# Performance work log

Measured on AMD Instinct MI355X. Metric: run time of the kernel, lower is better.

## Reference

```python
import jax, jax.numpy as jnp
import numpy as np

N = 100000
E = 1600000
F_IN, H = 64, 128


def setup_inputs() -> dict:
    key = jax.random.key(0)
    ks = jax.random.split(key, 8)
    inp = {
        "x": jax.random.normal(ks[0], (N, F_IN), dtype=jnp.float32),
        "edge_index": jax.random.randint(ks[1], (2, E), 0, N, dtype=jnp.int64),
        "W1": jax.random.normal(ks[2], (F_IN, H), dtype=jnp.float32) / np.sqrt(F_IN),
        "b1": jnp.zeros((H,), jnp.float32),
        "W2": jax.random.normal(ks[3], (H, H), dtype=jnp.float32) / np.sqrt(H),
        "b2": jnp.zeros((H,), jnp.float32),
        "W3": jax.random.normal(ks[4], (H, H // 2), dtype=jnp.float32) / np.sqrt(H),
        "b3": jnp.zeros((H // 2,), jnp.float32),
        "Wc1": jax.random.normal(ks[5], (H // 2, H // 4), dtype=jnp.float32) / np.sqrt(H // 2),
        "bc1": jnp.zeros((H // 4,), jnp.float32),
        "Wc2": jax.random.normal(ks[6], (H // 4, 2), dtype=jnp.float32) / np.sqrt(H // 4),
        "bc2": jnp.zeros((2,), jnp.float32),
    }
    return inp


def _gcn_norm(edge_index, n):
    # PyG GCNConv default: add self-loops, symmetric D^-1/2 A_hat D^-1/2 norm
    loop = jnp.arange(n, dtype=edge_index.dtype)
    src = jnp.concatenate([edge_index[0], loop])
    dst = jnp.concatenate([edge_index[1], loop])
    deg = jax.ops.segment_sum(jnp.ones_like(dst, dtype=jnp.float32), dst, num_segments=n)
    dis = jax.lax.rsqrt(jnp.maximum(deg, 1.0))
    norm = dis[src] * dis[dst]  # [E+N]
    return src, dst, norm


def _gcn_conv(x, W, b, src, dst, norm, n):
    h = x @ W                      # [N, H_out]
    msg = h[src] * norm[:, None]   # gather + scale, [E+N, H_out]
    out = jax.ops.segment_sum(msg, dst, num_segments=n)  # scatter-add
    return out + b


def reference(x, edge_index, W1, b1, W2, b2, W3, b3, Wc1, bc1, Wc2, bc2):
    n = x.shape[0]
    src, dst, norm = _gcn_norm(edge_index, n)
    h1 = jax.nn.relu(_gcn_conv(x, W1, b1, src, dst, norm, n))
    h2 = jax.nn.relu(_gcn_conv(h1, W2, b2, src, dst, norm, n))
    h3 = jax.nn.relu(_gcn_conv(h2, W3, b3, src, dst, norm, n))
    pooled = jnp.mean(h3, axis=0, keepdims=True)  # [1, H//2]
    z = jax.nn.relu(pooled @ Wc1 + bc1)
    logits = z @ Wc2 + bc2
    return jax.nn.softmax(logits, axis=1)
```

## Files before the change

kernel.cpp:

```cpp
#include <hip/hip_runtime.h>

#define NN 100000
#define NE 1600000
#define NBUCKET 391
#define CHUNK 4096

typedef __attribute__((ext_vector_type(2))) float v2f;
typedef __attribute__((ext_vector_type(8))) short bf16x8;
typedef __attribute__((ext_vector_type(4))) float f32x4;


__device__ __forceinline__ unsigned int pk4fp8(float a, float b, float c, float d) {
    int t = __builtin_amdgcn_cvt_pk_fp8_f32(a, b, 0, false);
    t = __builtin_amdgcn_cvt_pk_fp8_f32(c, d, t, true);
    return (unsigned int)t;
}
__device__ __forceinline__ void acc4(unsigned int u, float* a) {
    v2f p0 = __builtin_amdgcn_cvt_pk_f32_fp8((int)u, false);
    v2f p1 = __builtin_amdgcn_cvt_pk_f32_fp8((int)u, true);
    a[0] += p0.x; a[1] += p0.y; a[2] += p1.x; a[3] += p1.y;
}
__device__ __forceinline__ void acc16(uint4 u, float* a) {
    acc4(u.x, a); acc4(u.y, a + 4); acc4(u.z, a + 8); acc4(u.w, a + 12);
}


__device__ __forceinline__ unsigned short f2b(float f) {
    unsigned int u; __builtin_memcpy(&u, &f, 4);
    unsigned int r = (u + 0x7fffu + ((u >> 16) & 1u)) >> 16;
    return (unsigned short)r;
}
__device__ __forceinline__ unsigned int pk2b(float a, float b) {
    return (unsigned int)f2b(a) | ((unsigned int)f2b(b) << 16);
}

__global__ __launch_bounds__(256) void k_init(
    const float* __restrict__ W1, const float* __restrict__ W2,
    const float* __restrict__ W3, uint4* __restrict__ Wp,
    int* __restrict__ bcnt) {
    int t = blockIdx.x * 256 + threadIdx.x;
    if (t < 4096) {
        const float* W; int Dout, e, base;
        if (t < 1024)       { W = W1; Dout = 128; e = t;        base = 0; }
        else if (t < 3072)  { W = W2; Dout = 128; e = t - 1024; base = 1024; }
        else                { W = W3; Dout = 64;  e = t - 3072; base = 3072; }
        int k4q = e / Dout, ch = e % Dout;
        int k0 = (k4q >> 2) * 32 + (k4q & 3) * 8;
        float v[8];
        #pragma unroll
        for (int j = 0; j < 8; j++) v[j] = W[(k0 + j) * Dout + ch];
        uint4 u;
        u.x = pk2b(v[0], v[1]); u.y = pk2b(v[2], v[3]);
        u.z = pk2b(v[4], v[5]); u.w = pk2b(v[6], v[7]);
        Wp[base + e] = u;
    } else {
        int i = t - 4096;
        if (i < NBUCKET) bcnt[i] = 0;
    }
}


__global__ __launch_bounds__(256) void k_p1(const int* __restrict__ dst,
                                            int* __restrict__ bcnt, int E) {
    __shared__ int h[NBUCKET];
    for (int i = threadIdx.x; i < NBUCKET; i += 256) h[i] = 0;
    __syncthreads();
    int stride = gridDim.x * 256;
    for (int i = blockIdx.x * 256 + threadIdx.x; i < E; i += stride)
        atomicAdd(&h[dst[i] >> 8], 1);
    __syncthreads();
    for (int i = threadIdx.x; i < NBUCKET; i += 256)
        if (h[i]) atomicAdd(&bcnt[i], h[i]);
}

__global__ void k_scanb(const int* __restrict__ bcnt, int* __restrict__ bbase,
                        int* __restrict__ bfill) {
    __shared__ int s[512];
    int t = threadIdx.x;
    int v = (t < NBUCKET) ? bcnt[t] : 0;
    s[t] = v; __syncthreads();
    for (int off = 1; off < 512; off <<= 1) {
        int x = (t >= off) ? s[t - off] : 0;
        __syncthreads();
        s[t] += x;
        __syncthreads();
    }
    if (t < NBUCKET) { int ex = s[t] - v; bbase[t] = ex; bfill[t] = ex; }
    if (t == NBUCKET) bbase[t] = s[511];
}

__global__ __launch_bounds__(256) void k_p2(const int* __restrict__ src,
                                            const int* __restrict__ dst,
                                            int* __restrict__ bfill,
                                            unsigned int* __restrict__ entries, int E) {
    __shared__ int h[NBUCKET];
    __shared__ int cur[NBUCKET];
    int c0 = blockIdx.x * CHUNK;
    int c1 = min(E, c0 + CHUNK);
    for (int i = threadIdx.x; i < NBUCKET; i += 256) h[i] = 0;
    __syncthreads();
    for (int i = c0 + threadIdx.x; i < c1; i += 256) atomicAdd(&h[dst[i] >> 8], 1);
    __syncthreads();
    for (int i = threadIdx.x; i < NBUCKET; i += 256)
        cur[i] = h[i] ? atomicAdd(&bfill[i], h[i]) : 0;
    __syncthreads();
    for (int i = c0 + threadIdx.x; i < c1; i += 256) {
        int d = dst[i];
        int bkt = d >> 8;
        int pos = atomicAdd(&cur[bkt], 1);
        entries[pos] = (unsigned int)src[i] | ((unsigned int)(d & 255) << 17);
    }
}

__global__ __launch_bounds__(256) void k_p4x(const unsigned int* __restrict__ entries,
                                             const int* __restrict__ bbase,
                                             int* __restrict__ row_ptr,
                                             float* __restrict__ dis,
                                             int* __restrict__ col,
                                             const float4* __restrict__ x4,
                                             uint2* __restrict__ xb2, int N) {
    __shared__ int cnt[256];
    __shared__ int cur[256];
    __shared__ int sc[256];
    __shared__ float sdis[256];
    int b = blockIdx.x;
    int e0 = bbase[b], e1 = bbase[b + 1];
    int t = threadIdx.x;
    cnt[t] = 0; __syncthreads();
    for (int i = e0 + t; i < e1; i += 256)
        atomicAdd(&cnt[(entries[i] >> 17) & 255], 1);
    __syncthreads();
    int v = cnt[t];
    sc[t] = v; __syncthreads();
    for (int off = 1; off < 256; off <<= 1) {
        int x = (t >= off) ? sc[t - off] : 0;
        __syncthreads();
        sc[t] += x;
        __syncthreads();
    }
    int ex = sc[t] - v;
    int n = (b << 8) + t;
    float dv = rsqrtf((float)(v + 1));
    if (n <= N) row_ptr[n] = e0 + ex;
    if (n < N) dis[n] = dv;
    sdis[t] = dv;
    cur[t] = e0 + ex;
    __syncthreads();
    for (int i = e0 + t; i < e1; i += 256) {
        unsigned int en = entries[i];
        int pos = atomicAdd(&cur[(en >> 17) & 255], 1);
        col[pos] = (int)(en & 0x1FFFF);
    }
    for (int idx = t; idx < 256 * 8; idx += 256) {
        int node = idx >> 3, k = idx & 7;
        int gn = (b << 8) + node;
        if (gn < N) {
            float s = sdis[node];
            float4 A = x4[gn * 16 + 2 * k];
            float4 B = x4[gn * 16 + 2 * k + 1];
            uint2 u;
            u.x = pk4fp8(A.x * s, A.y * s, A.z * s, A.w * s);
            u.y = pk4fp8(B.x * s, B.y * s, B.z * s, B.w * s);
            xb2[gn * 8 + k] = u;
        }
    }
}

__global__ __launch_bounds__(256) void k_l1f(
    const uint4* __restrict__ xb4, const int* __restrict__ row_ptr,
    const int* __restrict__ col, const float* __restrict__ dis,
    const uint4* __restrict__ Wp, const float* __restrict__ b1,
    unsigned int* __restrict__ h1u, int N) {
    __shared__ unsigned short lds[4][16][72];
    const int tid = threadIdx.x, lane = tid & 63, wave = tid >> 6;
    const int slot = lane >> 2, seg = lane & 3;
    const int n = blockIdx.x * 64 + wave * 16 + slot;
    float a[16];
    #pragma unroll
    for (int q = 0; q < 16; q++) a[q] = 0.f;
    if (n < N) {
        int b = row_ptr[n], e = row_ptr[n + 1];
        acc16(xb4[n * 4 + seg], a);
        int i = b;
        for (; i + 4 <= e; i += 4) {
            int c0 = col[i], c1 = col[i + 1], c2 = col[i + 2], c3 = col[i + 3];
            uint4 u0 = xb4[c0 * 4 + seg], u1 = xb4[c1 * 4 + seg];
            uint4 u2 = xb4[c2 * 4 + seg], u3 = xb4[c3 * 4 + seg];
            acc16(u0, a); acc16(u1, a); acc16(u2, a); acc16(u3, a);
        }
        for (; i < e; i++) acc16(xb4[col[i] * 4 + seg], a);
        float s = dis[n];
        #pragma unroll
        for (int q = 0; q < 16; q++) a[q] *= s;
    }
    uint4 u0, u1;
    u0.x = pk2b(a[0],  a[1]);  u0.y = pk2b(a[2],  a[3]);
    u0.z = pk2b(a[4],  a[5]);  u0.w = pk2b(a[6],  a[7]);
    u1.x = pk2b(a[8],  a[9]);  u1.y = pk2b(a[10], a[11]);
    u1.z = pk2b(a[12], a[13]); u1.w = pk2b(a[14], a[15]);
    *(uint4*)&lds[wave][slot][seg * 16]     = u0;
    *(uint4*)&lds[wave][slot][seg * 16 + 8] = u1;
    __syncthreads();
    const int quad = lane >> 4, l16 = lane & 15;
    const int node = blockIdx.x * 64 + wave * 16 + l16;
    const bool valid = node < N;
    bf16x8 bfrag[2];
    #pragma unroll
    for (int kt = 0; kt < 2; kt++)
        bfrag[kt] = *(bf16x8*)&lds[wave][l16][kt * 32 + quad * 8];
    const float s2 = valid ? dis[node] : 0.f;
    #pragma unroll
    for (int ct = 0; ct < 8; ct++) {
        f32x4 c = {0.f, 0.f, 0.f, 0.f};
        #pragma unroll
        for (int kt = 0; kt < 2; kt++) {
            uint4 wu = Wp[(kt * 4 + quad) * 128 + ct * 16 + l16];
            c = __builtin_amdgcn_mfma_f32_16x16x32_bf16(*(bf16x8*)&wu, bfrag[kt], c, 0, 0, 0);
        }
        if (valid) {
            const int chb = ct * 16 + quad * 4;
            float r0 = fmaxf(c[0] + b1[chb + 0], 0.f) * s2;
            float r1 = fmaxf(c[1] + b1[chb + 1], 0.f) * s2;
            float r2 = fmaxf(c[2] + b1[chb + 2], 0.f) * s2;
            float r3 = fmaxf(c[3] + b1[chb + 3], 0.f) * s2;
            h1u[(size_t)node * 32 + ct * 4 + quad] = pk4fp8(r0, r1, r2, r3);
        }
    }
}

__global__ __launch_bounds__(256) void k_agg128s(
    const uint4* __restrict__ g4, const int* __restrict__ row_ptr,
    const int* __restrict__ col, const float* __restrict__ dis,
    uint4* __restrict__ outb, int N) {
    int tid = threadIdx.x;
    int lane = tid & 63, wave = tid >> 6;
    int slot = lane >> 3, seg = lane & 7;
    int n = blockIdx.x * 32 + wave * 8 + slot;
    if (n >= N) return;
    int b = row_ptr[n], e = row_ptr[n + 1];
    float a[16];
    #pragma unroll
    for (int q = 0; q < 16; q++) a[q] = 0.f;
    acc16(g4[n * 8 + seg], a);
    int i = b;
    for (; i + 4 <= e; i += 4) {
        int c0 = col[i], c1 = col[i + 1], c2 = col[i + 2], c3 = col[i + 3];
        uint4 u0 = g4[c0 * 8 + seg], u1 = g4[c1 * 8 + seg];
        uint4 u2 = g4[c2 * 8 + seg], u3 = g4[c3 * 8 + seg];
        acc16(u0, a); acc16(u1, a); acc16(u2, a); acc16(u3, a);
    }
    for (; i < e; i++) acc16(g4[col[i] * 8 + seg], a);
    float s = dis[n];
    uint4 u0, u1;
    u0.x = pk2b(s*a[0],  s*a[1]);  u0.y = pk2b(s*a[2],  s*a[3]);
    u0.z = pk2b(s*a[4],  s*a[5]);  u0.w = pk2b(s*a[6],  s*a[7]);
    u1.x = pk2b(s*a[8],  s*a[9]);  u1.y = pk2b(s*a[10], s*a[11]);
    u1.z = pk2b(s*a[12], s*a[13]); u1.w = pk2b(s*a[14], s*a[15]);
    outb[n * 16 + seg * 2]     = u0;
    outb[n * 16 + seg * 2 + 1] = u1;
}

__global__ __launch_bounds__(256) void k_mm23(
    const uint4* __restrict__ Xb,
    const uint4* __restrict__ Wp2, const uint4* __restrict__ Wp3,
    const float* __restrict__ b2, const float* __restrict__ dis,
    unsigned int* __restrict__ g3u, int N) {
    __shared__ unsigned short lds[4][16][136];
    const int tid = threadIdx.x, lane = tid & 63, wave = tid >> 6;
    const int quad = lane >> 4, l16 = lane & 15;
    const int node = blockIdx.x * 64 + wave * 16 + l16;
    const bool valid = node < N;
    const int nc = valid ? node : (N - 1);
    bf16x8 bfrag[4];
    const uint4* xrow = Xb + (size_t)nc * 16;
    #pragma unroll
    for (int kt = 0; kt < 4; kt++) {
        uint4 u = xrow[kt * 4 + quad];
        bfrag[kt] = *(bf16x8*)&u;
    }
    const float s = valid ? dis[node] : 0.f;
    #pragma unroll
    for (int ct = 0; ct < 8; ct++) {
        f32x4 c = {0.f, 0.f, 0.f, 0.f};
        #pragma unroll
        for (int kt = 0; kt < 4; kt++) {
            uint4 wu = Wp2[(kt * 4 + quad) * 128 + ct * 16 + l16];
            c = __builtin_amdgcn_mfma_f32_16x16x32_bf16(*(bf16x8*)&wu, bfrag[kt], c, 0, 0, 0);
        }
        const int chb = ct * 16 + quad * 4;
        float r0 = fmaxf(c[0] + b2[chb + 0], 0.f) * s;
        float r1 = fmaxf(c[1] + b2[chb + 1], 0.f) * s;
        float r2 = fmaxf(c[2] + b2[chb + 2], 0.f) * s;
        float r3 = fmaxf(c[3] + b2[chb + 3], 0.f) * s;
        uint2 u; u.x = pk2b(r0, r1); u.y = pk2b(r2, r3);
        *(uint2*)&lds[wave][l16][chb] = u;
    }
    __syncthreads();
    bf16x8 b2frag[4];
    #pragma unroll
    for (int kt = 0; kt < 4; kt++)
        b2frag[kt] = *(bf16x8*)&lds[wave][l16][kt * 32 + quad * 8];
    #pragma unroll
    for (int ct = 0; ct < 4; ct++) {
        f32x4 c = {0.f, 0.f, 0.f, 0.f};
        #pragma unroll
        for (int kt = 0; kt < 4; kt++) {
            uint4 wu = Wp3[(kt * 4 + quad) * 64 + ct * 16 + l16];
            c = __builtin_amdgcn_mfma_f32_16x16x32_bf16(*(bf16x8*)&wu, b2frag[kt], c, 0, 0, 0);
        }
        if (valid)
            g3u[(size_t)node * 16 + ct * 4 + quad] = pk4fp8(c[0], c[1], c[2], c[3]);
    }
}

__global__ __launch_bounds__(256) void k_aggpools(
    const uint4* __restrict__ g4, const int* __restrict__ row_ptr,
    const int* __restrict__ col, const float* __restrict__ dis,
    const float* __restrict__ b3, float* __restrict__ partial, int N) {
    int tid = threadIdx.x;
    int lane = tid & 63, wave = tid >> 6;
    int slot = lane >> 2, seg = lane & 3;
    int n = blockIdx.x * 64 + wave * 16 + slot;
    float ap[16];
    #pragma unroll
    for (int j = 0; j < 16; j++) ap[j] = 0.f;
    if (n < N) {
        int b = row_ptr[n], e = row_ptr[n + 1];
        float a[16];
        #pragma unroll
        for (int q = 0; q < 16; q++) a[q] = 0.f;
        acc16(g4[n * 4 + seg], a);
        int i = b;
        for (; i + 4 <= e; i += 4) {
            int c0 = col[i], c1 = col[i + 1], c2 = col[i + 2], c3 = col[i + 3];
            uint4 u0 = g4[c0 * 4 + seg], u1 = g4[c1 * 4 + seg];
            uint4 u2 = g4[c2 * 4 + seg], u3 = g4[c3 * 4 + seg];
            acc16(u0, a); acc16(u1, a); acc16(u2, a); acc16(u3, a);
        }
        for (; i < e; i++) acc16(g4[col[i] * 4 + seg], a);
        float s = dis[n];
        #pragma unroll
        for (int j = 0; j < 16; j++)
            ap[j] = fmaxf(s * a[j] + b3[seg * 16 + j], 0.f);
    }
    #pragma unroll
    for (int j = 0; j < 16; j++) {
        ap[j] += __shfl_xor(ap[j], 4);
        ap[j] += __shfl_xor(ap[j], 8);
        ap[j] += __shfl_xor(ap[j], 16);
        ap[j] += __shfl_xor(ap[j], 32);
    }
    __shared__ float red[4][64];
    if (slot == 0) {
        #pragma unroll
        for (int j = 0; j < 16; j++) red[wave][seg * 16 + j] = ap[j];
    }
    __syncthreads();
    if (tid < 64)
        partial[blockIdx.x * 64 + tid] =
            red[0][tid] + red[1][tid] + red[2][tid] + red[3][tid];
}

__global__ __launch_bounds__(256) void k_red(
    const float* __restrict__ partial, float* __restrict__ partial2, int NB) {
    int blk = blockIdx.x;
    int t = threadIdx.x;
    int lane = t & 63, grp = t >> 6;
    int start = blk * 16;
    int end = min(NB, start + 16);
    float s = 0.f;
    for (int b = start + grp; b < end; b += 4) s += partial[b * 64 + lane];
    __shared__ float red[256];
    red[t] = s; __syncthreads();
    if (t < 64)
        partial2[blk * 64 + t] = red[t] + red[t + 64] + red[t + 128] + red[t + 192];
}

__global__ __launch_bounds__(256) void k_head(
    const float* __restrict__ partial, const float* __restrict__ Wc1,
    const float* __restrict__ bc1, const float* __restrict__ Wc2,
    const float* __restrict__ bc2, float* __restrict__ out, int NB, float invN) {
    __shared__ float red[256];
    __shared__ float pooled[64];
    __shared__ float z[32];
    __shared__ float lg[2];
    int t = threadIdx.x;
    int lane = t & 63, grp = t >> 6;
    float s = 0.f;
    for (int b = grp; b < NB; b += 4) s += partial[b * 64 + lane];
    red[t] = s; __syncthreads();
    if (t < 64) pooled[t] = (red[t] + red[t + 64] + red[t + 128] + red[t + 192]) * invN;
    __syncthreads();
    if (t < 32) {
        float a = bc1[t];
        for (int l = 0; l < 64; l++) a += pooled[l] * Wc1[l * 32 + t];
        z[t] = fmaxf(a, 0.f);
    }
    __syncthreads();
    if (t < 2) {
        float a = bc2[t];
        for (int j = 0; j < 32; j++) a += z[j] * Wc2[j * 2 + t];
        lg[t] = a;
    }
    __syncthreads();
    if (t == 0) {
        float m = fmaxf(lg[0], lg[1]);
        float e0 = __expf(lg[0] - m), e1 = __expf(lg[1] - m);
        float inv = 1.f / (e0 + e1);
        out[0] = e0 * inv;
        out[1] = e1 * inv;
    }
}


extern "C" void kernel_launch(void* const* d_in, const int* in_sizes, int n_in,
                              void* d_out, int out_size, void* d_ws, size_t ws_size,
                              hipStream_t stream) {
    (void)in_sizes; (void)n_in; (void)out_size; (void)ws_size;
    const int N = NN, E = NE;

    const float* x   = (const float*)d_in[0];
    const int*   ei  = (const int*)d_in[1];
    const int*   srcp = ei;
    const int*   dstp = ei + E;
    const float* W1 = (const float*)d_in[2];
    const float* b1 = (const float*)d_in[3];
    const float* W2 = (const float*)d_in[4];
    const float* b2 = (const float*)d_in[5];
    const float* W3 = (const float*)d_in[6];
    const float* b3 = (const float*)d_in[7];
    const float* Wc1 = (const float*)d_in[8];
    const float* bc1 = (const float*)d_in[9];
    const float* Wc2 = (const float*)d_in[10];
    const float* bc2 = (const float*)d_in[11];
    float* out = (float*)d_out;

    char* base = (char*)d_ws;
    size_t off = 0;
    auto carve = [&](size_t bytes) -> char* {
        char* p = base + off;
        off = (off + bytes + 255) & ~(size_t)255;
        return p;
    };
    int*   bcnt    = (int*)carve((size_t)NBUCKET * 4);
    int*   bbase   = (int*)carve((size_t)(NBUCKET + 1) * 4);
    int*   bfill   = (int*)carve((size_t)NBUCKET * 4);
    int*   row_ptr = (int*)carve((size_t)(N + 1) * 4);
    int*   col     = (int*)carve((size_t)E * 4);
    float* dis     = (float*)carve((size_t)N * 4);
    float* partial = (float*)carve((size_t)1600 * 64 * 4);
    float* partial2= (float*)carve((size_t)128 * 64 * 4);
    uint4* Wp      = (uint4*)carve((size_t)4096 * 16);
    unsigned int* entries = (unsigned int*)carve((size_t)E * 4);
    unsigned int* xb      = (unsigned int*)carve((size_t)N * 64);
    unsigned int* h1u     = (unsigned int*)carve((size_t)N * 128);
    unsigned int* g3u     = (unsigned int*)carve((size_t)N * 64);
    uint4*        bufB    = (uint4*)carve((size_t)N * 128 * 2);

    k_init<<<18, 256, 0, stream>>>(W1, W2, W3, Wp, bcnt);
    k_p1<<<512, 256, 0, stream>>>(dstp, bcnt, E);
    k_scanb<<<1, 512, 0, stream>>>(bcnt, bbase, bfill);
    k_p2<<<(E + CHUNK - 1) / CHUNK, 256, 0, stream>>>(srcp, dstp, bfill, entries, E);
    k_p4x<<<NBUCKET, 256, 0, stream>>>(entries, bbase, row_ptr, dis, col,
                                       (const float4*)x, (uint2*)xb, N);

    const int NB64 = (N + 63) / 64;
    const int NB32 = (N + 31) / 32;

    k_l1f<<<NB64, 256, 0, stream>>>((const uint4*)xb, row_ptr, col, dis, Wp, b1, h1u, N);

    k_agg128s<<<NB32, 256, 0, stream>>>((const uint4*)h1u, row_ptr, col, dis, bufB, N);
    k_mm23<<<NB64, 256, 0, stream>>>(bufB, Wp + 1024, Wp + 3072, b2, dis, g3u, N);

    k_aggpools<<<NB64, 256, 0, stream>>>((const uint4*)g3u, row_ptr, col, dis, b3, partial, N);

    const int NRED = (NB64 + 15) / 16;
    k_red<<<NRED, 256, 0, stream>>>(partial, partial2, NB64);
    k_head<<<1, 256, 0, stream>>>(partial2, Wc1, bc1, Wc2, bc2, out, NRED, 1.0f / (float)N);
}
```

Measured before the change: 281.9 us.

## Fuse CSR build stages into one cooperative kernel and merge reduce with head

Merges the five CSR-construction kernels (weight packing, bucket histogram, bucket scan, bucket scatter, per-bucket sort plus fp8 packing of x) into a single cooperative kernel of 391 blocks that uses grid-wide syncs between phases. The final reduction and classifier head are also combined into one kernel, where the last finishing block does the head work through an atomic counter. The goal is to cut kernel launch overhead and gaps between dependent small kernels. In exchange the histogram and scatter passes run on only 391 blocks instead of 512 and 391, and the bucket scan becomes a serial loop in one thread.

Measured after the change: 480.4 us. 70.4% more time.

```diff
diff --git a/kernel.cpp b/kernel.cpp
--- a/kernel.cpp
+++ b/kernel.cpp
@@ -1,4 +1,7 @@
 #include <hip/hip_runtime.h>
+#include <hip/hip_cooperative_groups.h>
+
+namespace cg = cooperative_groups;
 
 #define NN 100000
 #define NE 1600000
@@ -34,16 +37,33 @@
     return (unsigned int)f2b(a) | ((unsigned int)f2b(b) << 16);
 }
 
-__global__ __launch_bounds__(256) void k_init(
+__global__ __launch_bounds__(256) void k_csr(
+    const int* __restrict__ src, const int* __restrict__ dst,
+    const float4* __restrict__ x4,
     const float* __restrict__ W1, const float* __restrict__ W2,
     const float* __restrict__ W3, uint4* __restrict__ Wp,
-    int* __restrict__ bcnt) {
-    int t = blockIdx.x * 256 + threadIdx.x;
-    if (t < 4096) {
+    int* __restrict__ bcnt, int* __restrict__ bbase, int* __restrict__ bfill,
+    int* __restrict__ row_ptr, float* __restrict__ dis, int* __restrict__ col,
+    unsigned int* __restrict__ entries, uint2* __restrict__ xb2,
+    int* __restrict__ done_cnt, int N, int E) {
+    cg::grid_group grid = cg::this_grid();
+    __shared__ int h[NBUCKET];
+    __shared__ int cur[NBUCKET];
+    __shared__ int scn[NBUCKET];
+    __shared__ int cnt4[256];
+    __shared__ int cur4[256];
+    __shared__ int sc4[256];
+    __shared__ float sdis[256];
+    const int b = blockIdx.x, t = threadIdx.x;
+    const int g = b * 256 + t;
+
+    if (g < NBUCKET) bcnt[g] = 0;
+    if (g == 0) *done_cnt = 0;
+    if (g < 4096) {
         const float* W; int Dout, e, base;
-        if (t < 1024)       { W = W1; Dout = 128; e = t;        base = 0; }
-        else if (t < 3072)  { W = W2; Dout = 128; e = t - 1024; base = 1024; }
-        else                { W = W3; Dout = 64;  e = t - 3072; base = 3072; }
+        if (g < 1024)       { W = W1; Dout = 128; e = g;        base = 0; }
+        else if (g < 3072)  { W = W2; Dout = 128; e = g - 1024; base = 1024; }
+        else                { W = W3; Dout = 64;  e = g - 3072; base = 3072; }
         int k4q = e / Dout, ch = e % Dout;
         int k0 = (k4q >> 2) * 32 + (k4q & 3) * 8;
         float v[8];
@@ -53,102 +73,73 @@
         u.x = pk2b(v[0], v[1]); u.y = pk2b(v[2], v[3]);
         u.z = pk2b(v[4], v[5]); u.w = pk2b(v[6], v[7]);
         Wp[base + e] = u;
-    } else {
-        int i = t - 4096;
-        if (i < NBUCKET) bcnt[i] = 0;
-    }
-}
-
-
-__global__ __launch_bounds__(256) void k_p1(const int* __restrict__ dst,
-                                            int* __restrict__ bcnt, int E) {
-    __shared__ int h[NBUCKET];
-    for (int i = threadIdx.x; i < NBUCKET; i += 256) h[i] = 0;
-    __syncthreads();
-    int stride = gridDim.x * 256;
-    for (int i = blockIdx.x * 256 + threadIdx.x; i < E; i += stride)
+    }
+    grid.sync();
+
+    for (int i = t; i < NBUCKET; i += 256) h[i] = 0;
+    __syncthreads();
+    for (int i = g; i < E; i += gridDim.x * 256)
         atomicAdd(&h[dst[i] >> 8], 1);
     __syncthreads();
-    for (int i = threadIdx.x; i < NBUCKET; i += 256)
+    for (int i = t; i < NBUCKET; i += 256)
         if (h[i]) atomicAdd(&bcnt[i], h[i]);
-}
-
-__global__ void k_scanb(const int* __restrict__ bcnt, int* __restrict__ bbase,
-                        int* __restrict__ bfill) {
-    __shared__ int s[512];
-    int t = threadIdx.x;
-    int v = (t < NBUCKET) ? bcnt[t] : 0;
-    s[t] = v; __syncthreads();
-    for (int off = 1; off < 512; off <<= 1) {
-        int x = (t >= off) ? s[t - off] : 0;
-        __syncthreads();
-        s[t] += x;
-        __syncthreads();
-    }
-    if (t < NBUCKET) { int ex = s[t] - v; bbase[t] = ex; bfill[t] = ex; }
-    if (t == NBUCKET) bbase[t] = s[511];
-}
-
-__global__ __launch_bounds__(256) void k_p2(const int* __restrict__ src,
-                                            const int* __restrict__ dst,
-                                            int* __restrict__ bfill,
-                                            unsigned int* __restrict__ entries, int E) {
-    __shared__ int h[NBUCKET];
-    __shared__ int cur[NBUCKET];
-    int c0 = blockIdx.x * CHUNK;
-    int c1 = min(E, c0 + CHUNK);
-    for (int i = threadIdx.x; i < NBUCKET; i += 256) h[i] = 0;
-    __syncthreads();
-    for (int i = c0 + threadIdx.x; i < c1; i += 256) atomicAdd(&h[dst[i] >> 8], 1);
-    __syncthreads();
-    for (int i = threadIdx.x; i < NBUCKET; i += 256)
-        cur[i] = h[i] ? atomicAdd(&bfill[i], h[i]) : 0;
-    __syncthreads();
-    for (int i = c0 + threadIdx.x; i < c1; i += 256) {
-        int d = dst[i];
-        int bkt = d >> 8;
-        int pos = atomicAdd(&cur[bkt], 1);
-        entries[pos] = (unsigned int)src[i] | ((unsigned int)(d & 255) << 17);
-    }
-}
-
-__global__ __launch_bounds__(256) void k_p4x(const unsigned int* __restrict__ entries,
-                                             const int* __restrict__ bbase,
-                                             int* __restrict__ row_ptr,
-                                             float* __restrict__ dis,
-                                             int* __restrict__ col,
-                                             const float4* __restrict__ x4,
-                                             uint2* __restrict__ xb2, int N) {
-    __shared__ int cnt[256];
-    __shared__ int cur[256];
-    __shared__ int sc[256];
-    __shared__ float sdis[256];
-    int b = blockIdx.x;
+    grid.sync();
+
+    if (b == 0) {
+        for (int i = t; i < NBUCKET; i += 256) scn[i] = bcnt[i];
+        __syncthreads();
+        if (t == 0) {
+            int run = 0;
+            for (int i = 0; i < NBUCKET; i++) { int v = scn[i]; scn[i] = run; run += v; }
+        }
+        __syncthreads();
+        for (int i = t; i < NBUCKET; i += 256) { bbase[i] = scn[i]; bfill[i] = scn[i]; }
+        if (t == 0) bbase[NBUCKET] = E;
+    }
+    grid.sync();
+
+    for (int cb = b; cb * CHUNK < E; cb += gridDim.x) {
+        int c0 = cb * CHUNK, c1 = min(E, c0 + CHUNK);
+        for (int i = t; i < NBUCKET; i += 256) h[i] = 0;
+        __syncthreads();
+        for (int i = c0 + t; i < c1; i += 256) atomicAdd(&h[dst[i] >> 8], 1);
+        __syncthreads();
+        for (int i = t; i < NBUCKET; i += 256)
+            cur[i] = h[i] ? atomicAdd(&bfill[i], h[i]) : 0;
+        __syncthreads();
+        for (int i = c0 + t; i < c1; i += 256) {
+            int d = dst[i];
+            int pos = atomicAdd(&cur[d >> 8], 1);
+            entries[pos] = (unsigned int)src[i] | ((unsigned int)(d & 255) << 17);
+        }
+        __syncthreads();
+    }
+    grid.sync();
+
     int e0 = bbase[b], e1 = bbase[b + 1];
-    int t = threadIdx.x;
-    cnt[t] = 0; __syncthreads();
+    cnt4[t] = 0; __syncthreads();
     for (int i = e0 + t; i < e1; i += 256)
-        atomicAdd(&cnt[(entries[i] >> 17) & 255], 1);
-    __syncthreads();
-    int v = cnt[t];
-    sc[t] = v; __syncthreads();
+        atomicAdd(&cnt4[(entries[i] >> 17) & 255], 1);
+    __syncthreads();
+    int v = cnt4[t];
+    sc4[t] = v; __syncthreads();
     for (int off = 1; off < 256; off <<= 1) {
-        int x = (t >= off) ? sc[t - off] : 0;
-        __syncthreads();
-        sc[t] += x;
-        __syncthreads();
-    }
-    int ex = sc[t] - v;
+        int x = (t >= off) ? sc4[t - off] : 0;
+        __syncthreads();
+        sc4[t] += x;
+        __syncthreads();
+    }
+    int ex = sc4[t] - v;
     int n = (b << 8) + t;
     float dv = rsqrtf((float)(v + 1));
     if (n <= N) row_ptr[n] = e0 + ex;
     if (n < N) dis[n] = dv;
     sdis[t] = dv;
-    cur[t] = e0 + ex;
+    cur4[t] = e0 + ex;
     __syncthreads();
     for (int i = e0 + t; i < e1; i += 256) {
         unsigned int en = entries[i];
-        int pos = atomicAdd(&cur[(en >> 17) & 255], 1);
+        int pos = atomicAdd(&cur4[(en >> 17) & 255], 1);
         col[pos] = (int)(en & 0x1FFFF);
     }
     for (int idx = t; idx < 256 * 8; idx += 256) {
@@ -361,34 +352,33 @@
             red[0][tid] + red[1][tid] + red[2][tid] + red[3][tid];
 }
 
-__global__ __launch_bounds__(256) void k_red(
-    const float* __restrict__ partial, float* __restrict__ partial2, int NB) {
-    int blk = blockIdx.x;
-    int t = threadIdx.x;
-    int lane = t & 63, grp = t >> 6;
-    int start = blk * 16;
-    int end = min(NB, start + 16);
-    float s = 0.f;
-    for (int b = start + grp; b < end; b += 4) s += partial[b * 64 + lane];
-    __shared__ float red[256];
-    red[t] = s; __syncthreads();
-    if (t < 64)
-        partial2[blk * 64 + t] = red[t] + red[t + 64] + red[t + 128] + red[t + 192];
-}
-
-__global__ __launch_bounds__(256) void k_head(
-    const float* __restrict__ partial, const float* __restrict__ Wc1,
-    const float* __restrict__ bc1, const float* __restrict__ Wc2,
-    const float* __restrict__ bc2, float* __restrict__ out, int NB, float invN) {
+__global__ __launch_bounds__(256) void k_redhead(
+    const float* __restrict__ partial, float* __restrict__ partial2,
+    const float* __restrict__ Wc1, const float* __restrict__ bc1,
+    const float* __restrict__ Wc2, const float* __restrict__ bc2,
+    float* __restrict__ out, int* __restrict__ done_cnt,
+    int NB, int NRED, float invN) {
     __shared__ float red[256];
     __shared__ float pooled[64];
     __shared__ float z[32];
     __shared__ float lg[2];
-    int t = threadIdx.x;
+    __shared__ int isLast;
+    int blk = blockIdx.x, t = threadIdx.x;
     int lane = t & 63, grp = t >> 6;
+    int start = blk * 16, end = min(NB, start + 16);
     float s = 0.f;
-    for (int b = grp; b < NB; b += 4) s += partial[b * 64 + lane];
+    for (int b = start + grp; b < end; b += 4) s += partial[b * 64 + lane];
     red[t] = s; __syncthreads();
+    if (t < 64)
+        partial2[blk * 64 + t] = red[t] + red[t + 64] + red[t + 128] + red[t + 192];
+    __threadfence();
+    if (t == 0) isLast = (atomicAdd(done_cnt, 1) == NRED - 1);
+    __syncthreads();
+    if (!isLast) return;
+    __threadfence();
+    float s2 = 0.f;
+    for (int b = grp; b < NRED; b += 4) s2 += partial2[b * 64 + lane];
+    red[t] = s2; __syncthreads();
     if (t < 64) pooled[t] = (red[t] + red[t + 64] + red[t + 128] + red[t + 192]) * invN;
     __syncthreads();
     if (t < 32) {
@@ -417,7 +407,7 @@
                               void* d_out, int out_size, void* d_ws, size_t ws_size,
                               hipStream_t stream) {
     (void)in_sizes; (void)n_in; (void)out_size; (void)ws_size;
-    const int N = NN, E = NE;
+    int N = NN, E = NE;
 
     const float* x   = (const float*)d_in[0];
     const int*   ei  = (const int*)d_in[1];
@@ -445,6 +435,7 @@
     int*   bcnt    = (int*)carve((size_t)NBUCKET * 4);
     int*   bbase   = (int*)carve((size_t)(NBUCKET + 1) * 4);
     int*   bfill   = (int*)carve((size_t)NBUCKET * 4);
+    int*   done_cnt= (int*)carve(256);
     int*   row_ptr = (int*)carve((size_t)(N + 1) * 4);
     int*   col     = (int*)carve((size_t)E * 4);
     float* dis     = (float*)carve((size_t)N * 4);
@@ -457,12 +448,18 @@
     unsigned int* g3u     = (unsigned int*)carve((size_t)N * 64);
     uint4*        bufB    = (uint4*)carve((size_t)N * 128 * 2);
 
-    k_init<<<18, 256, 0, stream>>>(W1, W2, W3, Wp, bcnt);
-    k_p1<<<512, 256, 0, stream>>>(dstp, bcnt, E);
-    k_scanb<<<1, 512, 0, stream>>>(bcnt, bbase, bfill);
-    k_p2<<<(E + CHUNK - 1) / CHUNK, 256, 0, stream>>>(srcp, dstp, bfill, entries, E);
-    k_p4x<<<NBUCKET, 256, 0, stream>>>(entries, bbase, row_ptr, dis, col,
-                                       (const float4*)x, (uint2*)xb, N);
+    const float4* x4 = (const float4*)x;
+    uint2* xb2 = (uint2*)xb;
+    void* args[] = {
+        (void*)&srcp, (void*)&dstp, (void*)&x4,
+        (void*)&W1, (void*)&W2, (void*)&W3, (void*)&Wp,
+        (void*)&bcnt, (void*)&bbase, (void*)&bfill,
+        (void*)&row_ptr, (void*)&dis, (void*)&col,
+        (void*)&entries, (void*)&xb2, (void*)&done_cnt,
+        (void*)&N, (void*)&E
+    };
+    hipLaunchCooperativeKernel((void*)k_csr, dim3(NBUCKET), dim3(256),
+                               args, 0, stream);
 
     const int NB64 = (N + 63) / 64;
     const int NB32 = (N + 31) / 32;
@@ -475,6 +472,6 @@
     k_aggpools<<<NB64, 256, 0, stream>>>((const uint4*)g3u, row_ptr, col, dis, b3, partial, N);
 
     const int NRED = (NB64 + 15) / 16;
-    k_red<<<NRED, 256, 0, stream>>>(partial, partial2, NB64);
-    k_head<<<1, 256, 0, stream>>>(partial2, Wc1, bc1, Wc2, bc2, out, NRED, 1.0f / (float)N);
-}
+    k_redhead<<<NRED, 256, 0, stream>>>(partial, partial2, Wc1, bc1, Wc2, bc2,
+                                        out, done_cnt, NB64, NRED, 1.0f / (float)N);
+}
```
